# Kernel tuning notes

Measured on AMD Instinct MI355X. Metric: run time of the kernel, lower is better.

Reference implementation:

```python
import jax, jax.numpy as jnp
import numpy as np

B, IN, H = 4096, 1024, 1024


def setup_inputs() -> dict:
    key = jax.random.key(0)
    ks = jax.random.split(key, 16)
    s = 1.0 / np.sqrt(IN)
    inp = {
        "x_t": jax.random.normal(ks[0], (B, IN), jnp.float32),
        "h_prev": jax.random.normal(ks[1], (B, H), jnp.float32),
        "c_prev": jax.random.normal(ks[2], (B, H), jnp.float32),
        "W_xi": jax.random.uniform(ks[3], (H, IN), jnp.float32, -s, s),
        "W_hi": jax.random.normal(ks[4], (H, H), jnp.float32) / np.sqrt(H),
        "b_i": jnp.zeros((H,), jnp.float32),
        "W_xf": jax.random.uniform(ks[5], (H, IN), jnp.float32, -s, s),
        "W_hf": jax.random.normal(ks[6], (H, H), jnp.float32) / np.sqrt(H),
        "b_f": jnp.ones((H,), jnp.float32),
        "W_xg": jax.random.uniform(ks[7], (H, IN), jnp.float32, -s, s),
        "W_hg": jax.random.normal(ks[8], (H, H), jnp.float32) / np.sqrt(H),
        "b_g": jnp.zeros((H,), jnp.float32),
        "W_xo": jax.random.uniform(ks[9], (H, IN), jnp.float32, -s, s),
        "W_ho": jax.random.normal(ks[10], (H, H), jnp.float32) / np.sqrt(H),
        "b_o": jnp.zeros((H,), jnp.float32),
    }
    return inp


def reference(x_t, h_prev, c_prev,
              W_xi, W_hi, b_i,
              W_xf, W_hf, b_f,
              W_xg, W_hg, b_g,
              W_xo, W_ho, b_o):
    # i/f/g/o gates: sigmoid/sigmoid/tanh/sigmoid of (x W_x^T + h W_h^T + b)
    i_t = jax.nn.sigmoid(x_t @ W_xi.T + h_prev @ W_hi.T + b_i)
    f_t = jax.nn.sigmoid(x_t @ W_xf.T + h_prev @ W_hf.T + b_f)
    g_t = jnp.tanh(x_t @ W_xg.T + h_prev @ W_hg.T + b_g)
    o_t = jax.nn.sigmoid(x_t @ W_xo.T + h_prev @ W_ho.T + b_o)
    c_t = f_t * c_prev + i_t * g_t
    h_t = o_t * jnp.tanh(c_t)
    return (h_t, c_t)
```

## Files before the change

kernel.cpp:

```cpp
#include <hip/hip_runtime.h>
#include <hip/hip_bf16.h>


constexpr int Mdim = 4096;
constexpr int Ndim = 4096;
constexpr int Kdim = 2048;
constexpr int Hdim = 1024;
constexpr int BM = 128;
constexpr int BN = 128;
constexpr int BK = 64;

using short8 = __attribute__((ext_vector_type(8))) short;
using f32x4  = __attribute__((ext_vector_type(4))) float;

__device__ __forceinline__ float sigmoid_(float x) {
    return 1.f / (1.f + __expf(-x));
}
__device__ __forceinline__ float tanh_(float x) {
    float e = __expf(2.f * x);
    return (e - 1.f) / (e + 1.f);
}

__global__ void build_A(const float* __restrict__ x, const float* __restrict__ h,
                        __hip_bfloat16* __restrict__ A) {
    int idx = blockIdx.x * 256 + threadIdx.x;
    int row = idx >> 8;
    int c8  = (idx & 255) * 8;
    const float* src = (c8 < 1024) ? (x + (size_t)row * 1024 + c8)
                                   : (h + (size_t)row * 1024 + (c8 - 1024));
    float4 f0 = ((const float4*)src)[0];
    float4 f1 = ((const float4*)src)[1];
    union { short8 v; __hip_bfloat16 e[8]; } u;
    u.e[0] = __float2bfloat16(f0.x); u.e[1] = __float2bfloat16(f0.y);
    u.e[2] = __float2bfloat16(f0.z); u.e[3] = __float2bfloat16(f0.w);
    u.e[4] = __float2bfloat16(f1.x); u.e[5] = __float2bfloat16(f1.y);
    u.e[6] = __float2bfloat16(f1.z); u.e[7] = __float2bfloat16(f1.w);
    *(short8*)(A + (size_t)row * Kdim + c8) = u.v;
}

__global__ void build_B(const float* __restrict__ Wxi, const float* __restrict__ Whi,
                        const float* __restrict__ Wxf, const float* __restrict__ Whf,
                        const float* __restrict__ Wxg, const float* __restrict__ Whg,
                        const float* __restrict__ Wxo, const float* __restrict__ Who,
                        __hip_bfloat16* __restrict__ B) {
    int idx = blockIdx.x * 256 + threadIdx.x;
    int n  = idx >> 8;
    int c8 = (idx & 255) * 8;
    int g = (n >> 4) & 3;
    int j = ((n >> 6) << 4) | (n & 15);
    const float* Wx = (g == 0) ? Wxi : (g == 1) ? Wxf : (g == 2) ? Wxg : Wxo;
    const float* Wh = (g == 0) ? Whi : (g == 1) ? Whf : (g == 2) ? Whg : Who;
    const float* src = (c8 < 1024) ? (Wx + (size_t)j * 1024 + c8)
                                   : (Wh + (size_t)j * 1024 + (c8 - 1024));
    float4 f0 = ((const float4*)src)[0];
    float4 f1 = ((const float4*)src)[1];
    union { short8 v; __hip_bfloat16 e[8]; } u;
    u.e[0] = __float2bfloat16(f0.x); u.e[1] = __float2bfloat16(f0.y);
    u.e[2] = __float2bfloat16(f0.z); u.e[3] = __float2bfloat16(f0.w);
    u.e[4] = __float2bfloat16(f1.x); u.e[5] = __float2bfloat16(f1.y);
    u.e[6] = __float2bfloat16(f1.z); u.e[7] = __float2bfloat16(f1.w);
    *(short8*)(B + (size_t)n * Kdim + c8) = u.v;
}

__launch_bounds__(256, 4)
__global__ void lstm_gemm(const __hip_bfloat16* __restrict__ A,
                          const __hip_bfloat16* __restrict__ B,
                          const float* __restrict__ c_prev,
                          const float* __restrict__ b_i, const float* __restrict__ b_f,
                          const float* __restrict__ b_g, const float* __restrict__ b_o,
                          float* __restrict__ out_h, float* __restrict__ out_c) {
    __shared__ __hip_bfloat16 As[BM * BK];
    __shared__ __hip_bfloat16 Bs[BN * BK];

    const int tid  = threadIdx.x;
    const int lane = tid & 63;
    const int w    = tid >> 6;
    const int wr   = w >> 1, wc = w & 1;
    const int l15  = lane & 15, lhi = lane >> 4;

    int bid = blockIdx.x;
    int swz = (bid & 7) * (1024 / 8) + (bid >> 3);
    const int bm = (swz >> 5) * BM;
    const int bn = (swz & 31) * BN;

    f32x4 acc[4][4];
#pragma unroll
    for (int a = 0; a < 4; ++a)
#pragma unroll
        for (int b = 0; b < 4; ++b)
            acc[a][b] = (f32x4){0.f, 0.f, 0.f, 0.f};

    for (int kt = 0; kt < Kdim; kt += BK) {
        __syncthreads();
#pragma unroll
        for (int it = 0; it < 4; ++it) {
            int off = it * 4096 + tid * 16;
            int row = off >> 7;
            int col = (off & 127) >> 1;
            __builtin_amdgcn_global_load_lds(
                (const __attribute__((address_space(1))) unsigned*)(A + (size_t)(bm + row) * Kdim + kt + col),
                (__attribute__((address_space(3))) unsigned*)((char*)As + off), 16, 0, 0);
            __builtin_amdgcn_global_load_lds(
                (const __attribute__((address_space(1))) unsigned*)(B + (size_t)(bn + row) * Kdim + kt + col),
                (__attribute__((address_space(3))) unsigned*)((char*)Bs + off), 16, 0, 0);
        }
        __syncthreads();

#pragma unroll
        for (int kk = 0; kk < 2; ++kk) {
            short8 af[4], bfr[4];
#pragma unroll
            for (int a = 0; a < 4; ++a)
                af[a] = *(const short8*)&As[(wr * 64 + a * 16 + l15) * BK + kk * 32 + lhi * 8];
#pragma unroll
            for (int b = 0; b < 4; ++b)
                bfr[b] = *(const short8*)&Bs[(wc * 64 + b * 16 + l15) * BK + kk * 32 + lhi * 8];
#pragma unroll
            for (int a = 0; a < 4; ++a)
#pragma unroll
                for (int b = 0; b < 4; ++b)
                    acc[a][b] = __builtin_amdgcn_mfma_f32_16x16x32_bf16(af[a], bfr[b], acc[a][b], 0, 0, 0);
        }
    }

    const int j0 = ((bn + wc * 64) >> 6) * 16 + l15;
    const float bi = b_i[j0];
    const float bf_ = b_f[j0];
    const float bg = b_g[j0];
    const float bo = b_o[j0];

#pragma unroll
    for (int a = 0; a < 4; ++a) {
        int mbase = bm + wr * 64 + a * 16 + lhi * 4;
#pragma unroll
        for (int r = 0; r < 4; ++r) {
            int m = mbase + r;
            float vi = acc[a][0][r] + bi;
            float vf = acc[a][1][r] + bf_;
            float vg = acc[a][2][r] + bg;
            float vo = acc[a][3][r] + bo;
            float it = sigmoid_(vi);
            float ft = sigmoid_(vf);
            float gt = tanh_(vg);
            float ot = sigmoid_(vo);
            float cp = c_prev[(size_t)m * Hdim + j0];
            float ct = ft * cp + it * gt;
            float ht = ot * tanh_(ct);
            out_h[(size_t)m * Hdim + j0] = ht;
            out_c[(size_t)m * Hdim + j0] = ct;
        }
    }
}

extern "C" void kernel_launch(void* const* d_in, const int* in_sizes, int n_in,
                              void* d_out, int out_size, void* d_ws, size_t ws_size,
                              hipStream_t stream) {
    const float* x_t    = (const float*)d_in[0];
    const float* h_prev = (const float*)d_in[1];
    const float* c_prev = (const float*)d_in[2];
    const float* W_xi   = (const float*)d_in[3];
    const float* W_hi   = (const float*)d_in[4];
    const float* b_i    = (const float*)d_in[5];
    const float* W_xf   = (const float*)d_in[6];
    const float* W_hf   = (const float*)d_in[7];
    const float* b_f    = (const float*)d_in[8];
    const float* W_xg   = (const float*)d_in[9];
    const float* W_hg   = (const float*)d_in[10];
    const float* b_g    = (const float*)d_in[11];
    const float* W_xo   = (const float*)d_in[12];
    const float* W_ho   = (const float*)d_in[13];
    const float* b_o    = (const float*)d_in[14];

    float* out_h = (float*)d_out;
    float* out_c = out_h + (size_t)Mdim * Hdim;

    __hip_bfloat16* Abf = (__hip_bfloat16*)d_ws;
    __hip_bfloat16* Bbf = Abf + (size_t)Mdim * Kdim;

    build_A<<<4096, 256, 0, stream>>>(x_t, h_prev, Abf);
    build_B<<<4096, 256, 0, stream>>>(W_xi, W_hi, W_xf, W_hf, W_xg, W_hg, W_xo, W_ho, Bbf);

    lstm_gemm<<<dim3((Mdim / BM) * (Ndim / BN)), 256, 0, stream>>>(
        Abf, Bbf, c_prev, b_i, b_f, b_g, b_o, out_h, out_c);
}
```

Baseline: 104.4 us.

## Use 256x256 tiles with 4-stage async LDS pipeline and XOR swizzle

Grows the GEMM block tile to 256x256 with 512 threads (8 waves, 128x64 per wave) and shrinks BK to 32. Global-to-LDS loads go through a 4-stage ring buffer with explicit vmcnt waits and a single barrier per k-step, so loads overlap MFMA work. The LDS layout is XOR-swizzled to avoid bank conflicts, and MFMA sections get raised wave priority. In exchange, occupancy drops to one block per CU, each wave holds more accumulator registers, and only 256 blocks are launched, which may leave some CUs underused.

```diff
diff --git a/kernel.cpp b/kernel.cpp
--- a/kernel.cpp
+++ b/kernel.cpp
@@ -6,9 +6,10 @@
 constexpr int Ndim = 4096;
 constexpr int Kdim = 2048;
 constexpr int Hdim = 1024;
-constexpr int BM = 128;
-constexpr int BN = 128;
-constexpr int BK = 64;
+constexpr int BM = 256;
+constexpr int BN = 256;
+constexpr int BK = 32;
+constexpr int NT = Kdim / BK;
 
 using short8 = __attribute__((ext_vector_type(8))) short;
 using f32x4  = __attribute__((ext_vector_type(4))) float;
@@ -62,76 +63,104 @@
     *(short8*)(B + (size_t)n * Kdim + c8) = u.v;
 }
 
-__launch_bounds__(256, 4)
+__launch_bounds__(512, 1)
 __global__ void lstm_gemm(const __hip_bfloat16* __restrict__ A,
                           const __hip_bfloat16* __restrict__ B,
                           const float* __restrict__ c_prev,
                           const float* __restrict__ b_i, const float* __restrict__ b_f,
                           const float* __restrict__ b_g, const float* __restrict__ b_o,
                           float* __restrict__ out_h, float* __restrict__ out_c) {
-    __shared__ __hip_bfloat16 As[BM * BK];
-    __shared__ __hip_bfloat16 Bs[BN * BK];
+    __shared__ __hip_bfloat16 lds[4][2][BM * BK];
 
     const int tid  = threadIdx.x;
     const int lane = tid & 63;
     const int w    = tid >> 6;
-    const int wr   = w >> 1, wc = w & 1;
+    const int wr   = w >> 2;
+    const int wc   = w & 3;
     const int l15  = lane & 15, lhi = lane >> 4;
 
     int bid = blockIdx.x;
-    int swz = (bid & 7) * (1024 / 8) + (bid >> 3);
-    const int bm = (swz >> 5) * BM;
-    const int bn = (swz & 31) * BN;
-
-    f32x4 acc[4][4];
-#pragma unroll
-    for (int a = 0; a < 4; ++a)
+    int swz = (bid & 7) * 32 + (bid >> 3);
+    const int bm = (swz >> 4) * BM;
+    const int bn = (swz & 15) * BN;
+
+    const int srow  = tid >> 2;
+    const int scole = (((tid & 3) * 16) ^ (((tid >> 2) & 6) << 3)) >> 1;
+
+    const int koff = (lhi * 16) ^ ((l15 & 6) << 3);
+
+#define STAGE(s, kt)                                                            \
+    do {                                                                        \
+        _Pragma("unroll")                                                       \
+        for (int i_ = 0; i_ < 2; ++i_)                                          \
+            __builtin_amdgcn_global_load_lds(                                   \
+                (const __attribute__((address_space(1))) unsigned*)(            \
+                    A + (size_t)(bm + i_ * 128 + srow) * Kdim + (kt) + scole),  \
+                (__attribute__((address_space(3))) unsigned*)(                  \
+                    (char*)&lds[s][0][0] + i_ * 8192 + tid * 16), 16, 0, 0);    \
+        _Pragma("unroll")                                                       \
+        for (int i_ = 0; i_ < 2; ++i_)                                          \
+            __builtin_amdgcn_global_load_lds(                                   \
+                (const __attribute__((address_space(1))) unsigned*)(            \
+                    B + (size_t)(bn + i_ * 128 + srow) * Kdim + (kt) + scole),  \
+                (__attribute__((address_space(3))) unsigned*)(                  \
+                    (char*)&lds[s][1][0] + i_ * 8192 + tid * 16), 16, 0, 0);    \
+    } while (0)
+
+    f32x4 acc[8][4];
+#pragma unroll
+    for (int a = 0; a < 8; ++a)
 #pragma unroll
         for (int b = 0; b < 4; ++b)
             acc[a][b] = (f32x4){0.f, 0.f, 0.f, 0.f};
 
-    for (int kt = 0; kt < Kdim; kt += BK) {
-        __syncthreads();
-#pragma unroll
-        for (int it = 0; it < 4; ++it) {
-            int off = it * 4096 + tid * 16;
-            int row = off >> 7;
-            int col = (off & 127) >> 1;
-            __builtin_amdgcn_global_load_lds(
-                (const __attribute__((address_space(1))) unsigned*)(A + (size_t)(bm + row) * Kdim + kt + col),
-                (__attribute__((address_space(3))) unsigned*)((char*)As + off), 16, 0, 0);
-            __builtin_amdgcn_global_load_lds(
-                (const __attribute__((address_space(1))) unsigned*)(B + (size_t)(bn + row) * Kdim + kt + col),
-                (__attribute__((address_space(3))) unsigned*)((char*)Bs + off), 16, 0, 0);
+    STAGE(0, 0);
+    STAGE(1, BK);
+    STAGE(2, 2 * BK);
+    asm volatile("s_waitcnt vmcnt(8)" ::: "memory");
+    __builtin_amdgcn_s_barrier();
+    __builtin_amdgcn_sched_barrier(0);
+
+    for (int t = 0; t < NT; ++t) {
+        if (t + 3 < NT) STAGE((t + 3) & 3, (t + 3) * BK);
+
+        const char* As = (const char*)&lds[t & 3][0][0];
+        const char* Bs = (const char*)&lds[t & 3][1][0];
+
+        short8 bfr[4];
+#pragma unroll
+        for (int b = 0; b < 4; ++b)
+            bfr[b] = *(const short8*)(Bs + (wc * 64 + b * 16 + l15) * 64 + koff);
+
+        __builtin_amdgcn_s_setprio(1);
+#pragma unroll
+        for (int a = 0; a < 8; ++a) {
+            short8 af = *(const short8*)(As + (wr * 128 + a * 16 + l15) * 64 + koff);
+#pragma unroll
+            for (int b = 0; b < 4; ++b)
+                acc[a][b] = __builtin_amdgcn_mfma_f32_16x16x32_bf16(af, bfr[b], acc[a][b], 0, 0, 0);
         }
-        __syncthreads();
-
-#pragma unroll
-        for (int kk = 0; kk < 2; ++kk) {
-            short8 af[4], bfr[4];
-#pragma unroll
-            for (int a = 0; a < 4; ++a)
-                af[a] = *(const short8*)&As[(wr * 64 + a * 16 + l15) * BK + kk * 32 + lhi * 8];
-#pragma unroll
-            for (int b = 0; b < 4; ++b)
-                bfr[b] = *(const short8*)&Bs[(wc * 64 + b * 16 + l15) * BK + kk * 32 + lhi * 8];
-#pragma unroll
-            for (int a = 0; a < 4; ++a)
-#pragma unroll
-                for (int b = 0; b < 4; ++b)
-                    acc[a][b] = __builtin_amdgcn_mfma_f32_16x16x32_bf16(af[a], bfr[b], acc[a][b], 0, 0, 0);
+        __builtin_amdgcn_s_setprio(0);
+
+        if (t < NT - 3)       asm volatile("s_waitcnt vmcnt(8)" ::: "memory");
+        else if (t == NT - 3) asm volatile("s_waitcnt vmcnt(4)" ::: "memory");
+        else if (t == NT - 2) asm volatile("s_waitcnt vmcnt(0)" ::: "memory");
+        if (t < NT - 1) {
+            __builtin_amdgcn_s_barrier();
+            __builtin_amdgcn_sched_barrier(0);
         }
     }
+#undef STAGE
 
     const int j0 = ((bn + wc * 64) >> 6) * 16 + l15;
-    const float bi = b_i[j0];
+    const float bi  = b_i[j0];
     const float bf_ = b_f[j0];
-    const float bg = b_g[j0];
-    const float bo = b_o[j0];
-
-#pragma unroll
-    for (int a = 0; a < 4; ++a) {
-        int mbase = bm + wr * 64 + a * 16 + lhi * 4;
+    const float bg  = b_g[j0];
+    const float bo  = b_o[j0];
+
+#pragma unroll
+    for (int a = 0; a < 8; ++a) {
+        int mbase = bm + wr * 128 + a * 16 + lhi * 4;
 #pragma unroll
         for (int r = 0; r < 4; ++r) {
             int m = mbase + r;
@@ -180,6 +209,6 @@
     build_A<<<4096, 256, 0, stream>>>(x_t, h_prev, Abf);
     build_B<<<4096, 256, 0, stream>>>(W_xi, W_hi, W_xf, W_hf, W_xg, W_hg, W_xo, W_ho, Bbf);
 
-    lstm_gemm<<<dim3((Mdim / BM) * (Ndim / BN)), 256, 0, stream>>>(
+    lstm_gemm<<<dim3((Mdim / BM) * (Ndim / BN)), 512, 0, stream>>>(
         Abf, Bbf, c_prev, b_i, b_f, b_g, b_o, out_h, out_c);
 }
```

After: 91.31 us. 12.5% less time.
